# Optimization experiments

Hardware: AMD Instinct MI355X
Metric: run time of the kernel (lower is better)

Reference implementation:

```python
import jax, jax.numpy as jnp
import numpy as np

K = 10
ALPHA = 0.1
N_NODES = 100000
N_EDGES = 1600000
D_FEAT = 50


def setup_inputs() -> dict:
    key = jax.random.key(0)
    k1, k2, k3 = jax.random.split(key, 3)
    feat = jax.random.normal(k1, (N_NODES, D_FEAT), dtype=jnp.float32)
    src = jax.random.randint(k2, (N_EDGES,), 0, N_NODES, dtype=jnp.int64)
    dst = jax.random.randint(k3, (N_EDGES,), 0, N_NODES, dtype=jnp.int64)
    return {"feat": feat, "src": src, "dst": dst}


def reference(feat, src, dst):
    # APPNP: H^{t+1} = (1-a) * D^{-1/2} A D^{-1/2} H^t + a * H^0
    n = feat.shape[0]
    # in-degree per node, clipped to >= 1 (as in the original clip_by_value)
    deg = jax.ops.segment_sum(jnp.ones(dst.shape[0], feat.dtype), dst, num_segments=n)
    norm = jnp.clip(deg, 1.0, None) ** -0.5  # [N]
    norm = norm[:, None]                      # broadcast over feature dims
    feat_0 = feat
    for _ in range(K):
        h = feat * norm                       # pre-normalize (D^{-1/2})
        # message = h[src] (edge weight is 1 since edge_drop=0), aggregate by sum at dst
        agg = jax.ops.segment_sum(h[src], dst, num_segments=n)  # [N, D]
        feat = (1.0 - ALPHA) * (agg * norm) + ALPHA * feat_0
    return feat
```

## Files before the change

kernel.cpp:

```cpp
#include <hip/hip_runtime.h>


#define NN 100000
#define EE 1600000
#define DD 50
#define GS 64
#define KK 10
#define NBLK 391
#define SLICES 32
#define RANGES 8
#define NR (NN / RANGES)
#define ES (EE / SLICES)

__device__ __forceinline__ float feat_at(const void* f, long long i, int ft) {
    if (ft) return ((const float*)f)[i];
    unsigned int w = ((unsigned int)((const unsigned short*)f)[i]) << 16;
    return __uint_as_float(w);
}

__device__ __forceinline__ float bf16_ld(const unsigned short* p, int i) {
    unsigned int w = ((unsigned int)p[i]) << 16;
    return __uint_as_float(w);
}

__device__ __forceinline__ unsigned short bf16_st(float x) {
    unsigned int u = __float_as_uint(x);
    unsigned int r = (u + 0x7FFF + ((u >> 16) & 1)) >> 16;
    return (unsigned short)r;
}

__global__ __launch_bounds__(512) void APPNPConv_62199716381208_build(
        const void* srcp, const void* dstp, unsigned int* counts,
        int* col_idx, const int* flag, int phase) {
    __shared__ unsigned int hist[NR];
    const int tid = threadIdx.x;
    const int r = blockIdx.x & 7;
    const int s = blockIdx.x >> 3;
    const int r0 = r * NR;
    const int is64 = flag[0];
    const long long e0 = (long long)s * ES;

    if (phase == 0) {
        for (int i = tid; i < NR; i += 512) hist[i] = 0u;
        __syncthreads();
        if (is64) {
            const longlong2* dp = (const longlong2*)((const long long*)dstp + e0);
            for (int i = tid; i < ES / 2; i += 512) {
                longlong2 dd = dp[i];
                unsigned int a = (unsigned int)((int)dd.x - r0);
                unsigned int b = (unsigned int)((int)dd.y - r0);
                if (a < (unsigned int)NR) atomicAdd(&hist[a], 1u);
                if (b < (unsigned int)NR) atomicAdd(&hist[b], 1u);
            }
        } else {
            const int2* dp = (const int2*)((const int*)dstp + e0);
            for (int i = tid; i < ES / 2; i += 512) {
                int2 dd = dp[i];
                unsigned int a = (unsigned int)(dd.x - r0);
                unsigned int b = (unsigned int)(dd.y - r0);
                if (a < (unsigned int)NR) atomicAdd(&hist[a], 1u);
                if (b < (unsigned int)NR) atomicAdd(&hist[b], 1u);
            }
        }
        __syncthreads();
        for (int i = tid; i < NR; i += 512)
            counts[(size_t)s * NN + r0 + i] = hist[i];
    } else {
        for (int i = tid; i < NR; i += 512)
            hist[i] = counts[(size_t)s * NN + r0 + i];
        __syncthreads();
        if (is64) {
            const longlong2* dp = (const longlong2*)((const long long*)dstp + e0);
            const longlong2* sp = (const longlong2*)((const long long*)srcp + e0);
            for (int i = tid; i < ES / 2; i += 512) {
                longlong2 dd = dp[i];
                longlong2 ss = sp[i];
                unsigned int a = (unsigned int)((int)dd.x - r0);
                unsigned int b = (unsigned int)((int)dd.y - r0);
                if (a < (unsigned int)NR) {
                    unsigned int pos = atomicAdd(&hist[a], 1u);
                    int c = (int)ss.x;
                    if (pos < (unsigned int)EE)
                        col_idx[pos] = ((unsigned int)c < (unsigned int)NN) ? c : 0;
                }
                if (b < (unsigned int)NR) {
                    unsigned int pos = atomicAdd(&hist[b], 1u);
                    int c = (int)ss.y;
                    if (pos < (unsigned int)EE)
                        col_idx[pos] = ((unsigned int)c < (unsigned int)NN) ? c : 0;
                }
            }
        } else {
            const int2* dp = (const int2*)((const int*)dstp + e0);
            const int2* sp = (const int2*)((const int*)srcp + e0);
            for (int i = tid; i < ES / 2; i += 512) {
                int2 dd = dp[i];
                int2 ss = sp[i];
                unsigned int a = (unsigned int)(dd.x - r0);
                unsigned int b = (unsigned int)(dd.y - r0);
                if (a < (unsigned int)NR) {
                    unsigned int pos = atomicAdd(&hist[a], 1u);
                    if (pos < (unsigned int)EE)
                        col_idx[pos] = ((unsigned int)ss.x < (unsigned int)NN) ? ss.x : 0;
                }
                if (b < (unsigned int)NR) {
                    unsigned int pos = atomicAdd(&hist[b], 1u);
                    if (pos < (unsigned int)EE)
                        col_idx[pos] = ((unsigned int)ss.y < (unsigned int)NN) ? ss.y : 0;
                }
            }
        }
    }
}

__global__ __launch_bounds__(512) void APPNPConv_62199716381208_kernel(
        const void* featp, const void* srcp, const void* dstp,
        int* deg, float* norm, int* row_ptr, int* col_idx, int* bsum, int* flag,
        unsigned int* counts,
        const unsigned short* gin, unsigned short* gout, float* outp,
        int phase, int last) {
    __shared__ int sh[512];
    const int tid = threadIdx.x;

    if (phase == 0) {
        if (blockIdx.x == 0 && tid == 0) {
            const int* a = (const int*)dstp;
            int odd_or = a[1] | a[3] | a[5] | a[7] | a[9] | a[11] | a[13] | a[15];
            flag[0] = (odd_or == 0) ? 1 : 0;
            const unsigned short* w = (const unsigned short*)featp;
            int isf32 = 0;
            for (int k = 0; k < 64; ++k) {
                unsigned int b = ((unsigned int)w[k]) << 16;
                float ax = fabsf(__uint_as_float(b));
                if (!(ax < 100.0f)) isf32 = 1;
            }
            flag[1] = isf32;
        }
        return;
    }
    if (phase == 2) {
        int n = blockIdx.x * 256 + tid;
        int total = 0;
        if (n < NN) {
            #pragma unroll 4
            for (int s = 0; s < SLICES; ++s)
                total += (int)counts[(size_t)s * NN + n];
            deg[n] = total;
            norm[n] = rsqrtf((float)(total < 1 ? 1 : total));
        }
        sh[tid] = total;
        __syncthreads();
        for (int off = 128; off > 0; off >>= 1) {
            if (tid < off) sh[tid] += sh[tid + off];
            __syncthreads();
        }
        if (tid == 0) bsum[blockIdx.x] = sh[0];
        return;
    }
    if (phase == 3) {
        int v = (tid < NBLK) ? bsum[tid] : 0;
        sh[tid] = v;
        __syncthreads();
        for (int off = 1; off < 512; off <<= 1) {
            int x = (tid >= off) ? sh[tid - off] : 0;
            __syncthreads();
            sh[tid] += x;
            __syncthreads();
        }
        if (tid < NBLK) bsum[tid] = sh[tid] - v;
        return;
    }
    if (phase == 4) {
        int i = blockIdx.x * 256 + tid;
        int v = (i < NN) ? deg[i] : 0;
        sh[tid] = v;
        __syncthreads();
        for (int off = 1; off < 256; off <<= 1) {
            int x = (tid >= off) ? sh[tid - off] : 0;
            __syncthreads();
            sh[tid] += x;
            __syncthreads();
        }
        int excl = sh[tid] - v + bsum[blockIdx.x];
        if (i < NN) {
            row_ptr[i] = excl;
            unsigned int run = (unsigned int)excl;
            for (int s = 0; s < SLICES; ++s) {
                size_t o = (size_t)s * NN + i;
                unsigned int c = counts[o];
                counts[o] = run;
                run += c;
            }
        }
        if (i == 0) row_ptr[NN] = EE;
        return;
    }
    if (phase == 6) {
        int gidx = blockIdx.x * 256 + tid;
        int v = gidx >> 6;
        int d = gidx & 63;
        if (v < NN && d < DD) {
            float x = feat_at(featp, (long long)v * DD + d, flag[1]);
            gout[v * GS + d] = bf16_st(x * norm[v]);
        }
        return;
    }
    {
        const int lane = tid & 63;
        const int v = (blockIdx.x << 2) + (tid >> 6);
        if (v >= NN) return;
        const int beg = row_ptr[v];
        const int end = row_ptr[v + 1];
        const int act = (lane < DD);
        float s0 = 0.0f, s1 = 0.0f, s2 = 0.0f, s3 = 0.0f;
        for (int base = beg; base < end; base += 64) {
            int idx = base + lane;
            int my = (idx < end) ? col_idx[idx] : 0;
            int cnt = end - base;
            if (cnt > 64) cnt = 64;
            int j = 0;
            for (; j + 16 <= cnt; j += 16) {
                int c0  = __shfl(my, j,      64);
                int c1  = __shfl(my, j + 1,  64);
                int c2  = __shfl(my, j + 2,  64);
                int c3  = __shfl(my, j + 3,  64);
                int c4  = __shfl(my, j + 4,  64);
                int c5  = __shfl(my, j + 5,  64);
                int c6  = __shfl(my, j + 6,  64);
                int c7  = __shfl(my, j + 7,  64);
                int c8  = __shfl(my, j + 8,  64);
                int c9  = __shfl(my, j + 9,  64);
                int c10 = __shfl(my, j + 10, 64);
                int c11 = __shfl(my, j + 11, 64);
                int c12 = __shfl(my, j + 12, 64);
                int c13 = __shfl(my, j + 13, 64);
                int c14 = __shfl(my, j + 14, 64);
                int c15 = __shfl(my, j + 15, 64);
                if (act) {
                    float v0  = bf16_ld(gin, c0  * GS + lane);
                    float v1  = bf16_ld(gin, c1  * GS + lane);
                    float v2  = bf16_ld(gin, c2  * GS + lane);
                    float v3  = bf16_ld(gin, c3  * GS + lane);
                    float v4  = bf16_ld(gin, c4  * GS + lane);
                    float v5  = bf16_ld(gin, c5  * GS + lane);
                    float v6  = bf16_ld(gin, c6  * GS + lane);
                    float v7  = bf16_ld(gin, c7  * GS + lane);
                    float v8  = bf16_ld(gin, c8  * GS + lane);
                    float v9  = bf16_ld(gin, c9  * GS + lane);
                    float v10 = bf16_ld(gin, c10 * GS + lane);
                    float v11 = bf16_ld(gin, c11 * GS + lane);
                    float v12 = bf16_ld(gin, c12 * GS + lane);
                    float v13 = bf16_ld(gin, c13 * GS + lane);
                    float v14 = bf16_ld(gin, c14 * GS + lane);
                    float v15 = bf16_ld(gin, c15 * GS + lane);
                    s0 += (v0 + v4) + (v8 + v12);
                    s1 += (v1 + v5) + (v9 + v13);
                    s2 += (v2 + v6) + (v10 + v14);
                    s3 += (v3 + v7) + (v11 + v15);
                }
            }
            for (; j + 8 <= cnt; j += 8) {
                int c0 = __shfl(my, j, 64);
                int c1 = __shfl(my, j + 1, 64);
                int c2 = __shfl(my, j + 2, 64);
                int c3 = __shfl(my, j + 3, 64);
                int c4 = __shfl(my, j + 4, 64);
                int c5 = __shfl(my, j + 5, 64);
                int c6 = __shfl(my, j + 6, 64);
                int c7 = __shfl(my, j + 7, 64);
                if (act) {
                    float v0 = bf16_ld(gin, c0 * GS + lane);
                    float v1 = bf16_ld(gin, c1 * GS + lane);
                    float v2 = bf16_ld(gin, c2 * GS + lane);
                    float v3 = bf16_ld(gin, c3 * GS + lane);
                    float v4 = bf16_ld(gin, c4 * GS + lane);
                    float v5 = bf16_ld(gin, c5 * GS + lane);
                    float v6 = bf16_ld(gin, c6 * GS + lane);
                    float v7 = bf16_ld(gin, c7 * GS + lane);
                    s0 += v0 + v4;
                    s1 += v1 + v5;
                    s2 += v2 + v6;
                    s3 += v3 + v7;
                }
            }
            for (; j + 4 <= cnt; j += 4) {
                int c0 = __shfl(my, j, 64);
                int c1 = __shfl(my, j + 1, 64);
                int c2 = __shfl(my, j + 2, 64);
                int c3 = __shfl(my, j + 3, 64);
                if (act) {
                    s0 += bf16_ld(gin, c0 * GS + lane);
                    s1 += bf16_ld(gin, c1 * GS + lane);
                    s2 += bf16_ld(gin, c2 * GS + lane);
                    s3 += bf16_ld(gin, c3 * GS + lane);
                }
            }
            for (; j < cnt; ++j) {
                int c = __shfl(my, j, 64);
                if (act) s0 += bf16_ld(gin, c * GS + lane);
            }
        }
        if (act) {
            float sum = (s0 + s1) + (s2 + s3);
            float nv = norm[v];
            float f0 = feat_at(featp, (long long)v * DD + lane, flag[1]);
            float res = 0.9f * (sum * nv) + 0.1f * f0;
            if (last) outp[v * DD + lane] = res;
            else      gout[v * GS + lane] = bf16_st(res * nv);
        }
    }
}

extern "C" void kernel_launch(void* const* d_in, const int* in_sizes, int n_in,
                              void* d_out, int out_size, void* d_ws, size_t ws_size,
                              hipStream_t stream) {
    const void* featp = d_in[0];
    const void* src = d_in[1];
    const void* dst = d_in[2];
    float* outf = (float*)d_out;
    unsigned short* outb16 = (unsigned short*)d_out;
    unsigned int* counts = (unsigned int*)d_out;
    size_t out_bytes = (size_t)out_size * 4;
    (void)in_sizes;

    if (n_in != 3) {
        hipMemsetAsync(d_out, 0x50, out_bytes, stream);
        return;
    }

    size_t a_deg  = (((size_t)NN * 4) + 255) / 256 * 256;
    size_t a_norm = a_deg;
    size_t a_rp   = (((size_t)(NN + 1) * 4) + 255) / 256 * 256;
    size_t a_col  = (((size_t)EE * 4) + 255) / 256 * 256;
    size_t a_bsum = (((size_t)NBLK * 4) + 255) / 256 * 256;
    size_t a_flag = 256;
    size_t a_buf  = (((size_t)NN * GS * 2) + 255) / 256 * 256;
    if (ws_size < a_deg + a_norm + a_rp + a_col + a_bsum + a_flag + a_buf ||
        out_bytes < (size_t)SLICES * NN * 4) {
        hipMemsetAsync(d_out, 0x40, out_bytes, stream);
        return;
    }
    char* p = (char*)d_ws;
    int* deg      = (int*)p;   p += a_deg;
    float* norm   = (float*)p; p += a_norm;
    int* row_ptr  = (int*)p;   p += a_rp;
    int* col_idx  = (int*)p;   p += a_col;
    int* bsum     = (int*)p;   p += a_bsum;
    int* flag     = (int*)p;   p += a_flag;
    unsigned short* bufA = (unsigned short*)p;

    (void)hipGetLastError();

    #define LCH(grid, blk, gi, go, ph, la) \
        APPNPConv_62199716381208_kernel<<<(grid), (blk), 0, stream>>>( \
            featp, src, dst, deg, norm, row_ptr, col_idx, bsum, flag, counts, \
            (gi), (go), outf, (ph), (la))
    #define LCB(ph) \
        APPNPConv_62199716381208_build<<<SLICES * RANGES, 512, 0, stream>>>( \
            src, dst, counts, col_idx, flag, (ph))

    LCH(1, 256, bufA, bufA, 0, 0);
    LCB(0);
    LCH(NBLK, 256, bufA, bufA, 2, 0);
    LCH(1, 512, bufA, bufA, 3, 0);
    LCH(NBLK, 256, bufA, bufA, 4, 0);
    LCB(1);
    LCH((NN * GS + 255) / 256, 256, bufA, outb16, 6, 0);

    for (int it = 1; it <= KK; ++it) {
        const unsigned short* gi = (it & 1) ? outb16 : bufA;
        unsigned short* go       = (it & 1) ? bufA : outb16;
        LCH(NN / 4, 256, gi, go, 7, (it == KK) ? 1 : 0);
    }
    #undef LCH
    #undef LCB

    if (hipGetLastError() != hipSuccess) {
        hipMemsetAsync(d_out, 0xBF, out_bytes, stream);
    }
}
```

Baseline: 661.2 us.

## Pack bf16 feature rows densely, cache bf16 feat0, widen build loads, fold flag kernel

Shrinks the bf16 ping-pong row stride from 64 to 50 elements, so each gathered row covers fewer bytes and cache lines. It also stores a bf16 copy of the initial features in the output buffer, so iterations read 2-byte instead of 4-byte residuals. The CSR build kernels now load four indices per thread per iteration, and the separate dtype-detection kernel is merged into the first build launch. Nontemporal loads are used for col_idx. Rows of 100 bytes are no longer aligned to cache lines, which may cost some gather efficiency, and the residual term gains extra bf16 rounding.

```diff
diff --git a/kernel.cpp b/kernel.cpp
--- a/kernel.cpp
+++ b/kernel.cpp
@@ -4,7 +4,6 @@
 #define NN 100000
 #define EE 1600000
 #define DD 50
-#define GS 64
 #define KK 10
 #define NBLK 391
 #define SLICES 32
@@ -30,103 +29,20 @@
 }
 
 __global__ __launch_bounds__(512) void APPNPConv_62199716381208_build(
-        const void* srcp, const void* dstp, unsigned int* counts,
-        int* col_idx, const int* flag, int phase) {
+        const void* srcp, const void* dstp, const void* featp,
+        unsigned int* counts, int* col_idx, int* flag, int phase) {
     __shared__ unsigned int hist[NR];
     const int tid = threadIdx.x;
     const int r = blockIdx.x & 7;
     const int s = blockIdx.x >> 3;
     const int r0 = r * NR;
-    const int is64 = flag[0];
     const long long e0 = (long long)s * ES;
 
     if (phase == 0) {
-        for (int i = tid; i < NR; i += 512) hist[i] = 0u;
-        __syncthreads();
-        if (is64) {
-            const longlong2* dp = (const longlong2*)((const long long*)dstp + e0);
-            for (int i = tid; i < ES / 2; i += 512) {
-                longlong2 dd = dp[i];
-                unsigned int a = (unsigned int)((int)dd.x - r0);
-                unsigned int b = (unsigned int)((int)dd.y - r0);
-                if (a < (unsigned int)NR) atomicAdd(&hist[a], 1u);
-                if (b < (unsigned int)NR) atomicAdd(&hist[b], 1u);
-            }
-        } else {
-            const int2* dp = (const int2*)((const int*)dstp + e0);
-            for (int i = tid; i < ES / 2; i += 512) {
-                int2 dd = dp[i];
-                unsigned int a = (unsigned int)(dd.x - r0);
-                unsigned int b = (unsigned int)(dd.y - r0);
-                if (a < (unsigned int)NR) atomicAdd(&hist[a], 1u);
-                if (b < (unsigned int)NR) atomicAdd(&hist[b], 1u);
-            }
-        }
-        __syncthreads();
-        for (int i = tid; i < NR; i += 512)
-            counts[(size_t)s * NN + r0 + i] = hist[i];
-    } else {
-        for (int i = tid; i < NR; i += 512)
-            hist[i] = counts[(size_t)s * NN + r0 + i];
-        __syncthreads();
-        if (is64) {
-            const longlong2* dp = (const longlong2*)((const long long*)dstp + e0);
-            const longlong2* sp = (const longlong2*)((const long long*)srcp + e0);
-            for (int i = tid; i < ES / 2; i += 512) {
-                longlong2 dd = dp[i];
-                longlong2 ss = sp[i];
-                unsigned int a = (unsigned int)((int)dd.x - r0);
-                unsigned int b = (unsigned int)((int)dd.y - r0);
-                if (a < (unsigned int)NR) {
-                    unsigned int pos = atomicAdd(&hist[a], 1u);
-                    int c = (int)ss.x;
-                    if (pos < (unsigned int)EE)
-                        col_idx[pos] = ((unsigned int)c < (unsigned int)NN) ? c : 0;
-                }
-                if (b < (unsigned int)NR) {
-                    unsigned int pos = atomicAdd(&hist[b], 1u);
-                    int c = (int)ss.y;
-                    if (pos < (unsigned int)EE)
-                        col_idx[pos] = ((unsigned int)c < (unsigned int)NN) ? c : 0;
-                }
-            }
-        } else {
-            const int2* dp = (const int2*)((const int*)dstp + e0);
-            const int2* sp = (const int2*)((const int*)srcp + e0);
-            for (int i = tid; i < ES / 2; i += 512) {
-                int2 dd = dp[i];
-                int2 ss = sp[i];
-                unsigned int a = (unsigned int)(dd.x - r0);
-                unsigned int b = (unsigned int)(dd.y - r0);
-                if (a < (unsigned int)NR) {
-                    unsigned int pos = atomicAdd(&hist[a], 1u);
-                    if (pos < (unsigned int)EE)
-                        col_idx[pos] = ((unsigned int)ss.x < (unsigned int)NN) ? ss.x : 0;
-                }
-                if (b < (unsigned int)NR) {
-                    unsigned int pos = atomicAdd(&hist[b], 1u);
-                    if (pos < (unsigned int)EE)
-                        col_idx[pos] = ((unsigned int)ss.y < (unsigned int)NN) ? ss.y : 0;
-                }
-            }
-        }
-    }
-}
-
-__global__ __launch_bounds__(512) void APPNPConv_62199716381208_kernel(
-        const void* featp, const void* srcp, const void* dstp,
-        int* deg, float* norm, int* row_ptr, int* col_idx, int* bsum, int* flag,
-        unsigned int* counts,
-        const unsigned short* gin, unsigned short* gout, float* outp,
-        int phase, int last) {
-    __shared__ int sh[512];
-    const int tid = threadIdx.x;
-
-    if (phase == 0) {
+        const int* a = (const int*)dstp;
+        const int is64 = ((a[1] | a[3] | a[5] | a[7] | a[9] | a[11] | a[13] | a[15]) == 0);
         if (blockIdx.x == 0 && tid == 0) {
-            const int* a = (const int*)dstp;
-            int odd_or = a[1] | a[3] | a[5] | a[7] | a[9] | a[11] | a[13] | a[15];
-            flag[0] = (odd_or == 0) ? 1 : 0;
+            flag[0] = is64;
             const unsigned short* w = (const unsigned short*)featp;
             int isf32 = 0;
             for (int k = 0; k < 64; ++k) {
@@ -136,8 +52,125 @@
             }
             flag[1] = isf32;
         }
-        return;
-    }
+        for (int i = tid; i < NR; i += 512) hist[i] = 0u;
+        __syncthreads();
+        if (is64) {
+            const longlong2* dp = (const longlong2*)((const long long*)dstp + e0);
+            for (int i = tid; i < ES / 4; i += 512) {
+                longlong2 d0 = dp[2 * i];
+                longlong2 d1 = dp[2 * i + 1];
+                unsigned int a0 = (unsigned int)((int)d0.x - r0);
+                unsigned int a1 = (unsigned int)((int)d0.y - r0);
+                unsigned int a2 = (unsigned int)((int)d1.x - r0);
+                unsigned int a3 = (unsigned int)((int)d1.y - r0);
+                if (a0 < (unsigned int)NR) atomicAdd(&hist[a0], 1u);
+                if (a1 < (unsigned int)NR) atomicAdd(&hist[a1], 1u);
+                if (a2 < (unsigned int)NR) atomicAdd(&hist[a2], 1u);
+                if (a3 < (unsigned int)NR) atomicAdd(&hist[a3], 1u);
+            }
+        } else {
+            const int4* dp = (const int4*)((const int*)dstp + e0);
+            for (int i = tid; i < ES / 4; i += 512) {
+                int4 dd = dp[i];
+                unsigned int a0 = (unsigned int)(dd.x - r0);
+                unsigned int a1 = (unsigned int)(dd.y - r0);
+                unsigned int a2 = (unsigned int)(dd.z - r0);
+                unsigned int a3 = (unsigned int)(dd.w - r0);
+                if (a0 < (unsigned int)NR) atomicAdd(&hist[a0], 1u);
+                if (a1 < (unsigned int)NR) atomicAdd(&hist[a1], 1u);
+                if (a2 < (unsigned int)NR) atomicAdd(&hist[a2], 1u);
+                if (a3 < (unsigned int)NR) atomicAdd(&hist[a3], 1u);
+            }
+        }
+        __syncthreads();
+        for (int i = tid; i < NR; i += 512)
+            counts[(size_t)s * NN + r0 + i] = hist[i];
+    } else {
+        const int is64 = flag[0];
+        for (int i = tid; i < NR; i += 512)
+            hist[i] = counts[(size_t)s * NN + r0 + i];
+        __syncthreads();
+        if (is64) {
+            const longlong2* dp = (const longlong2*)((const long long*)dstp + e0);
+            const longlong2* sp = (const longlong2*)((const long long*)srcp + e0);
+            for (int i = tid; i < ES / 4; i += 512) {
+                longlong2 d0 = dp[2 * i];
+                longlong2 d1 = dp[2 * i + 1];
+                longlong2 s0 = sp[2 * i];
+                longlong2 s1 = sp[2 * i + 1];
+                unsigned int a0 = (unsigned int)((int)d0.x - r0);
+                unsigned int a1 = (unsigned int)((int)d0.y - r0);
+                unsigned int a2 = (unsigned int)((int)d1.x - r0);
+                unsigned int a3 = (unsigned int)((int)d1.y - r0);
+                if (a0 < (unsigned int)NR) {
+                    unsigned int pos = atomicAdd(&hist[a0], 1u);
+                    int c = (int)s0.x;
+                    if (pos < (unsigned int)EE)
+                        col_idx[pos] = ((unsigned int)c < (unsigned int)NN) ? c : 0;
+                }
+                if (a1 < (unsigned int)NR) {
+                    unsigned int pos = atomicAdd(&hist[a1], 1u);
+                    int c = (int)s0.y;
+                    if (pos < (unsigned int)EE)
+                        col_idx[pos] = ((unsigned int)c < (unsigned int)NN) ? c : 0;
+                }
+                if (a2 < (unsigned int)NR) {
+                    unsigned int pos = atomicAdd(&hist[a2], 1u);
+                    int c = (int)s1.x;
+                    if (pos < (unsigned int)EE)
+                        col_idx[pos] = ((unsigned int)c < (unsigned int)NN) ? c : 0;
+                }
+                if (a3 < (unsigned int)NR) {
+                    unsigned int pos = atomicAdd(&hist[a3], 1u);
+                    int c = (int)s1.y;
+                    if (pos < (unsigned int)EE)
+                        col_idx[pos] = ((unsigned int)c < (unsigned int)NN) ? c : 0;
+                }
+            }
+        } else {
+            const int4* dp = (const int4*)((const int*)dstp + e0);
+            const int4* sp = (const int4*)((const int*)srcp + e0);
+            for (int i = tid; i < ES / 4; i += 512) {
+                int4 dd = dp[i];
+                int4 ss = sp[i];
+                unsigned int a0 = (unsigned int)(dd.x - r0);
+                unsigned int a1 = (unsigned int)(dd.y - r0);
+                unsigned int a2 = (unsigned int)(dd.z - r0);
+                unsigned int a3 = (unsigned int)(dd.w - r0);
+                if (a0 < (unsigned int)NR) {
+                    unsigned int pos = atomicAdd(&hist[a0], 1u);
+                    if (pos < (unsigned int)EE)
+                        col_idx[pos] = ((unsigned int)ss.x < (unsigned int)NN) ? ss.x : 0;
+                }
+                if (a1 < (unsigned int)NR) {
+                    unsigned int pos = atomicAdd(&hist[a1], 1u);
+                    if (pos < (unsigned int)EE)
+                        col_idx[pos] = ((unsigned int)ss.y < (unsigned int)NN) ? ss.y : 0;
+                }
+                if (a2 < (unsigned int)NR) {
+                    unsigned int pos = atomicAdd(&hist[a2], 1u);
+                    if (pos < (unsigned int)EE)
+                        col_idx[pos] = ((unsigned int)ss.z < (unsigned int)NN) ? ss.z : 0;
+                }
+                if (a3 < (unsigned int)NR) {
+                    unsigned int pos = atomicAdd(&hist[a3], 1u);
+                    if (pos < (unsigned int)EE)
+                        col_idx[pos] = ((unsigned int)ss.w < (unsigned int)NN) ? ss.w : 0;
+                }
+            }
+        }
+    }
+}
+
+__global__ __launch_bounds__(512) void APPNPConv_62199716381208_kernel(
+        const void* featp, const void* srcp, const void* dstp,
+        int* deg, float* norm, int* row_ptr, int* col_idx, int* bsum, int* flag,
+        unsigned int* counts, unsigned short* f0b,
+        const unsigned short* gin, unsigned short* gout, float* outp,
+        int phase, int last) {
+    __shared__ int sh[512];
+    const int tid = threadIdx.x;
+
     if (phase == 2) {
         int n = blockIdx.x * 256 + tid;
         int total = 0;
@@ -196,12 +229,12 @@
         return;
     }
     if (phase == 6) {
-        int gidx = blockIdx.x * 256 + tid;
-        int v = gidx >> 6;
-        int d = gidx & 63;
-        if (v < NN && d < DD) {
-            float x = feat_at(featp, (long long)v * DD + d, flag[1]);
-            gout[v * GS + d] = bf16_st(x * norm[v]);
+        int i = blockIdx.x * 256 + tid;
+        if (i < NN * DD) {
+            int v = i / DD;
+            float x = feat_at(featp, i, flag[1]);
+            gout[i] = bf16_st(x * norm[v]);
+            f0b[i] = bf16_st(x);
         }
         return;
     }
@@ -215,7 +248,7 @@
         float s0 = 0.0f, s1 = 0.0f, s2 = 0.0f, s3 = 0.0f;
         for (int base = beg; base < end; base += 64) {
             int idx = base + lane;
-            int my = (idx < end) ? col_idx[idx] : 0;
+            int my = (idx < end) ? __builtin_nontemporal_load(col_idx + idx) : 0;
             int cnt = end - base;
             if (cnt > 64) cnt = 64;
             int j = 0;
@@ -237,22 +270,22 @@
                 int c14 = __shfl(my, j + 14, 64);
                 int c15 = __shfl(my, j + 15, 64);
                 if (act) {
-                    float v0  = bf16_ld(gin, c0  * GS + lane);
-                    float v1  = bf16_ld(gin, c1  * GS + lane);
-                    float v2  = bf16_ld(gin, c2  * GS + lane);
-                    float v3  = bf16_ld(gin, c3  * GS + lane);
-                    float v4  = bf16_ld(gin, c4  * GS + lane);
-                    float v5  = bf16_ld(gin, c5  * GS + lane);
-                    float v6  = bf16_ld(gin, c6  * GS + lane);
-                    float v7  = bf16_ld(gin, c7  * GS + lane);
-                    float v8  = bf16_ld(gin, c8  * GS + lane);
-                    float v9  = bf16_ld(gin, c9  * GS + lane);
-                    float v10 = bf16_ld(gin, c10 * GS + lane);
-                    float v11 = bf16_ld(gin, c11 * GS + lane);
-                    float v12 = bf16_ld(gin, c12 * GS + lane);
-                    float v13 = bf16_ld(gin, c13 * GS + lane);
-                    float v14 = bf16_ld(gin, c14 * GS + lane);
-                    float v15 = bf16_ld(gin, c15 * GS + lane);
+                    float v0  = bf16_ld(gin, c0  * DD + lane);
+                    float v1  = bf16_ld(gin, c1  * DD + lane);
+                    float v2  = bf16_ld(gin, c2  * DD + lane);
+                    float v3  = bf16_ld(gin, c3  * DD + lane);
+                    float v4  = bf16_ld(gin, c4  * DD + lane);
+                    float v5  = bf16_ld(gin, c5  * DD + lane);
+                    float v6  = bf16_ld(gin, c6  * DD + lane);
+                    float v7  = bf16_ld(gin, c7  * DD + lane);
+                    float v8  = bf16_ld(gin, c8  * DD + lane);
+                    float v9  = bf16_ld(gin, c9  * DD + lane);
+                    float v10 = bf16_ld(gin, c10 * DD + lane);
+                    float v11 = bf16_ld(gin, c11 * DD + lane);
+                    float v12 = bf16_ld(gin, c12 * DD + lane);
+                    float v13 = bf16_ld(gin, c13 * DD + lane);
+                    float v14 = bf16_ld(gin, c14 * DD + lane);
+                    float v15 = bf16_ld(gin, c15 * DD + lane);
                     s0 += (v0 + v4) + (v8 + v12);
                     s1 += (v1 + v5) + (v9 + v13);
                     s2 += (v2 + v6) + (v10 + v14);
@@ -269,14 +302,14 @@
                 int c6 = __shfl(my, j + 6, 64);
                 int c7 = __shfl(my, j + 7, 64);
                 if (act) {
-                    float v0 = bf16_ld(gin, c0 * GS + lane);
-                    float v1 = bf16_ld(gin, c1 * GS + lane);
-                    float v2 = bf16_ld(gin, c2 * GS + lane);
-                    float v3 = bf16_ld(gin, c3 * GS + lane);
-                    float v4 = bf16_ld(gin, c4 * GS + lane);
-                    float v5 = bf16_ld(gin, c5 * GS + lane);
-                    float v6 = bf16_ld(gin, c6 * GS + lane);
-                    float v7 = bf16_ld(gin, c7 * GS + lane);
+                    float v0 = bf16_ld(gin, c0 * DD + lane);
+                    float v1 = bf16_ld(gin, c1 * DD + lane);
+                    float v2 = bf16_ld(gin, c2 * DD + lane);
+                    float v3 = bf16_ld(gin, c3 * DD + lane);
+                    float v4 = bf16_ld(gin, c4 * DD + lane);
+                    float v5 = bf16_ld(gin, c5 * DD + lane);
+                    float v6 = bf16_ld(gin, c6 * DD + lane);
+                    float v7 = bf16_ld(gin, c7 * DD + lane);
                     s0 += v0 + v4;
                     s1 += v1 + v5;
                     s2 += v2 + v6;
@@ -289,24 +322,28 @@
                 int c2 = __shfl(my, j + 2, 64);
                 int c3 = __shfl(my, j + 3, 64);
                 if (act) {
-                    s0 += bf16_ld(gin, c0 * GS + lane);
-                    s1 += bf16_ld(gin, c1 * GS + lane);
-                    s2 += bf16_ld(gin, c2 * GS + lane);
-                    s3 += bf16_ld(gin, c3 * GS + lane);
+                    s0 += bf16_ld(gin, c0 * DD + lane);
+                    s1 += bf16_ld(gin, c1 * DD + lane);
+                    s2 += bf16_ld(gin, c2 * DD + lane);
+                    s3 += bf16_ld(gin, c3 * DD + lane);
                 }
             }
             for (; j < cnt; ++j) {
                 int c = __shfl(my, j, 64);
-                if (act) s0 += bf16_ld(gin, c * GS + lane);
+                if (act) s0 += bf16_ld(gin, c * DD + lane);
             }
         }
         if (act) {
             float sum = (s0 + s1) + (s2 + s3);
             float nv = norm[v];
-            float f0 = feat_at(featp, (long long)v * DD + lane, flag[1]);
-            float res = 0.9f * (sum * nv) + 0.1f * f0;
-            if (last) outp[v * DD + lane] = res;
-            else      gout[v * GS + lane] = bf16_st(res * nv);
+            if (last) {
+                float f0 = feat_at(featp, (long long)v * DD + lane, flag[1]);
+                outp[v * DD + lane] = 0.9f * (sum * nv) + 0.1f * f0;
+            } else {
+                float f0 = bf16_ld(f0b, v * DD + lane);
+                float res = 0.9f * (sum * nv) + 0.1f * f0;
+                gout[v * DD + lane] = bf16_st(res * nv);
+            }
         }
     }
 }
@@ -318,7 +355,8 @@
     const void* src = d_in[1];
     const void* dst = d_in[2];
     float* outf = (float*)d_out;
-    unsigned short* outb16 = (unsigned short*)d_out;
+    unsigned short* P_do = (unsigned short*)d_out;
+    unsigned short* f0b  = (unsigned short*)d_out + (size_t)NN * DD;
     unsigned int* counts = (unsigned int*)d_out;
     size_t out_bytes = (size_t)out_size * 4;
     (void)in_sizes;
@@ -334,8 +372,9 @@
     size_t a_col  = (((size_t)EE * 4) + 255) / 256 * 256;
     size_t a_bsum = (((size_t)NBLK * 4) + 255) / 256 * 256;
     size_t a_flag = 256;
-    size_t a_buf  = (((size_t)NN * GS * 2) + 255) / 256 * 256;
+    size_t a_buf  = (((size_t)NN * DD * 2) + 255) / 256 * 256;
     if (ws_size < a_deg + a_norm + a_rp + a_col + a_bsum + a_flag + a_buf ||
+        out_bytes < (size_t)NN * DD * 4 ||
         out_bytes < (size_t)SLICES * NN * 4) {
         hipMemsetAsync(d_out, 0x40, out_bytes, stream);
         return;
@@ -347,29 +386,28 @@
     int* col_idx  = (int*)p;   p += a_col;
     int* bsum     = (int*)p;   p += a_bsum;
     int* flag     = (int*)p;   p += a_flag;
-    unsigned short* bufA = (unsigned short*)p;
+    unsigned short* P_ws = (unsigned short*)p;
 
     (void)hipGetLastError();
 
     #define LCH(grid, blk, gi, go, ph, la) \
         APPNPConv_62199716381208_kernel<<<(grid), (blk), 0, stream>>>( \
             featp, src, dst, deg, norm, row_ptr, col_idx, bsum, flag, counts, \
-            (gi), (go), outf, (ph), (la))
+            f0b, (gi), (go), outf, (ph), (la))
     #define LCB(ph) \
         APPNPConv_62199716381208_build<<<SLICES * RANGES, 512, 0, stream>>>( \
-            src, dst, counts, col_idx, flag, (ph))
-
-    LCH(1, 256, bufA, bufA, 0, 0);
+            src, dst, featp, counts, col_idx, flag, (ph))
+
     LCB(0);
-    LCH(NBLK, 256, bufA, bufA, 2, 0);
-    LCH(1, 512, bufA, bufA, 3, 0);
-    LCH(NBLK, 256, bufA, bufA, 4, 0);
+    LCH(NBLK, 256, P_ws, P_ws, 2, 0);
+    LCH(1, 512, P_ws, P_ws, 3, 0);
+    LCH(NBLK, 256, P_ws, P_ws, 4, 0);
     LCB(1);
-    LCH((NN * GS + 255) / 256, 256, bufA, outb16, 6, 0);
+    LCH((NN * DD + 255) / 256, 256, P_ws, P_do, 6, 0);
 
     for (int it = 1; it <= KK; ++it) {
-        const unsigned short* gi = (it & 1) ? outb16 : bufA;
-        unsigned short* go       = (it & 1) ? bufA : outb16;
+        const unsigned short* gi = (it & 1) ? P_do : P_ws;
+        unsigned short* go       = (it & 1) ? P_ws : P_do;
         LCH(NN / 4, 256, gi, go, 7, (it == KK) ? 1 : 0);
     }
     #undef LCH
```

Result: no change. 666.5 us (+0.8%).
